# Kernel optimization log

Hardware: AMD Instinct MI355X
Metric: run time of the kernel (lower is better)

Reference implementation:

```python
import jax, jax.numpy as jnp
import numpy as np

LAMBDA1 = 0.3366
LAMBDA2 = 0.2424
LAMBDA3 = 0.06
LR = 0.1
N_ITERS = 10          # fixed iteration count standing in for the eps-based while loop
BETA1, BETA2, ADAM_EPS = 0.9, 0.999, 1e-8


def setup_inputs() -> dict:
    key = jax.random.key(0)
    k1, k2, k3 = jax.random.split(key, 3)
    D, T, K = 512, 50000, 16
    return {
        "embedding": jax.random.normal(k1, (D, T), jnp.float32),
        "basis_init": jax.random.normal(k2, (D, K), jnp.float32),
        "activation_init": jax.random.normal(k3, (K, T), jnp.float32),
        "k": K,
    }


def _matrix_l1(X):
    # torch.linalg.norm(X, ord=1) on a 2D tensor = induced 1-norm = max column abs-sum
    return jnp.max(jnp.sum(jnp.abs(X), axis=0))


def _jitter(A):
    # temporal jitter penalty: sum of abs frame-to-frame differences
    return jnp.sum(jnp.abs(A[:, 1:] - A[:, :-1]))


def _shrink(X):
    # faithful to the (buggy) torch _shrink: sign(X) * max(0, |X - lr*l|)
    return jnp.sign(X) * jnp.maximum(0.0, jnp.abs(X - LR * LAMBDA1))


def _adam(p, g, m, v, t):
    m = BETA1 * m + (1.0 - BETA1) * g
    v = BETA2 * v + (1.0 - BETA2) * g * g
    mh = m / (1.0 - BETA1 ** t)
    vh = v / (1.0 - BETA2 ** t)
    p = p - LR * mh / (jnp.sqrt(vh) + ADAM_EPS)
    return p, m, v


def _run(embedding, basis_init, activation_init):
    A = activation_init  # optimizer_act.step() is never called in the source -> A is constant

    def loss_from_B(B):
        return (_matrix_l1(embedding - B @ A)
                + LAMBDA1 * _matrix_l1(B)
                + LAMBDA2 * _matrix_l1(A)
                + LAMBDA3 * _jitter(A))

    # iteration 1: loss is computed on the raw parameter (shrink applied after the step)
    P = basis_init
    m = jnp.zeros_like(P)
    v = jnp.zeros_like(P)
    g = jax.grad(loss_from_B)(P)
    P, m, v = _adam(P, g, m, v, jnp.float32(1.0))

    # iterations 2..N: loss sees shrink(P); gradient flows through the shrink into P
    def step(carry, t):
        P, m, v = carry
        g = jax.grad(lambda p: loss_from_B(_shrink(p)))(P)
        P, m, v = _adam(P, g, m, v, t)
        return (P, m, v), None

    ts = jnp.arange(2, N_ITERS + 1, dtype=jnp.float32)
    (P, m, v), _ = jax.lax.scan(step, (P, m, v), ts)
    return _shrink(P), A


def reference(embedding, basis_init, activation_init, k):
    # returns (embedding_basis_matrix, activation_matrix) as in OutputDiarization
    return _run(embedding, basis_init, activation_init)
```

## Files before the change

### kernel.cpp

```cpp
#include <hip/hip_runtime.h>

#define D 512
#define T 50000
#define K 16

#define ROWS_PER_SLICE 64
#define N_SLICES (D / ROWS_PER_SLICE)

#define LAMBDA1 0.3366f
#define LR      0.1f
#define SHRINK_C (LR * LAMBDA1)
#define BETA1   0.9f
#define BETA2   0.999f
#define ADAM_EPS 1e-8f

__device__ __forceinline__ float sgn(float x) {
    return (x > 0.f) ? 1.f : ((x < 0.f) ? -1.f : 0.f);
}

__global__ void init_kernel(const float* __restrict__ Pin, float* __restrict__ P,
                            float* __restrict__ m, float* __restrict__ v,
                            float* __restrict__ B, unsigned long long* slot) {
    int idx = blockIdx.x * blockDim.x + threadIdx.x;
    if (idx < D * K) {
        float p = Pin[idx];
        P[idx] = p;
        m[idx] = 0.f;
        v[idx] = 0.f;
        B[idx] = p;
    }
    if (idx == 0) *slot = 0ull;
}

__global__ __launch_bounds__(256) void partial_colsum_kernel(
        const float* __restrict__ E, const float* __restrict__ A,
        const float* __restrict__ B, float* __restrict__ partial) {
    int j = blockIdx.x * blockDim.x + threadIdx.x;
    int s = blockIdx.y;
    if (j >= T) return;

    float a[K];
#pragma unroll
    for (int k = 0; k < K; ++k) a[k] = A[k * T + j];

    int r0 = s * ROWS_PER_SLICE;
    float acc = 0.f;
#pragma unroll 4
    for (int ii = 0; ii < ROWS_PER_SLICE; ++ii) {
        int i = r0 + ii;
        float r = E[i * T + j];
        const float* Br = B + i * K;
#pragma unroll
        for (int k = 0; k < K; ++k) r -= Br[k] * a[k];
        acc += fabsf(r);
    }
    partial[s * T + j] = acc;
}

__global__ __launch_bounds__(256) void reduce_argmax_kernel(
        const float* __restrict__ partial, unsigned long long* slot) {
    int j = blockIdx.x * blockDim.x + threadIdx.x;
    float acc = 0.f;
    if (j < T) {
#pragma unroll
        for (int s = 0; s < N_SLICES; ++s) acc += partial[s * T + j];
    }
    unsigned long long key =
        (((unsigned long long)__float_as_uint(acc)) << 32) | (unsigned int)j;
    if (j >= T) key = 0ull;

#pragma unroll
    for (int off = 32; off > 0; off >>= 1) {
        unsigned long long o = __shfl_down(key, off, 64);
        if (o > key) key = o;
    }
    __shared__ unsigned long long wmax[4];
    int lane = threadIdx.x & 63, wid = threadIdx.x >> 6;
    if (lane == 0) wmax[wid] = key;
    __syncthreads();
    if (threadIdx.x == 0) {
        unsigned long long best = wmax[0];
        for (int w = 1; w < 4; ++w)
            if (wmax[w] > best) best = wmax[w];
        atomicMax(slot, best);
    }
}

__global__ __launch_bounds__(512) void update_kernel(
        const float* __restrict__ E, const float* __restrict__ A,
        float* __restrict__ B, float* __restrict__ P,
        float* __restrict__ m, float* __restrict__ v,
        unsigned long long* slot, float bias1, float bias2, int shrinkGrad) {
    int i = threadIdx.x;
    __shared__ float colB[K];
    __shared__ int js_s, ks_s;
    if (i < K) colB[i] = 0.f;
    if (i == 0) js_s = (int)((*slot) & 0xffffffffull);
    __syncthreads();
    int js = js_s;

    float b[K];
#pragma unroll
    for (int k = 0; k < K; ++k) b[k] = B[i * K + k];

    float r = E[i * T + js];
#pragma unroll
    for (int k = 0; k < K; ++k) r -= b[k] * A[k * T + js];
    float s = sgn(r);

#pragma unroll
    for (int k = 0; k < K; ++k) {
        float x = fabsf(b[k]);
#pragma unroll
        for (int off = 32; off > 0; off >>= 1) x += __shfl_down(x, off, 64);
        if ((threadIdx.x & 63) == 0) atomicAdd(&colB[k], x);
    }
    __syncthreads();
    if (i == 0) {
        int kb = 0;
        float best = colB[0];
        for (int k = 1; k < K; ++k)
            if (colB[k] > best) { best = colB[k]; kb = k; }
        ks_s = kb;
        *slot = 0ull;
    }
    __syncthreads();
    int ks = ks_s;

#pragma unroll
    for (int k = 0; k < K; ++k) {
        float g = -s * A[k * T + js];
        if (k == ks) g += LAMBDA1 * sgn(b[k]);
        float p = P[i * K + k];
        if (shrinkGrad) g *= sgn(p) * sgn(p - SHRINK_C);
        float mm = BETA1 * m[i * K + k] + (1.f - BETA1) * g;
        float vv = BETA2 * v[i * K + k] + (1.f - BETA2) * g * g;
        m[i * K + k] = mm;
        v[i * K + k] = vv;
        p -= LR * (mm / bias1) / (sqrtf(vv / bias2) + ADAM_EPS);
        P[i * K + k] = p;
        B[i * K + k] = sgn(p) * fmaxf(0.f, fabsf(p - SHRINK_C));
    }
}

__global__ void output_kernel(const float* __restrict__ B, const float* __restrict__ A,
                              float4* __restrict__ out) {
    int idx = blockIdx.x * blockDim.x + threadIdx.x;
    const int nB4 = (D * K) / 4;
    const int nTot4 = (D * K + K * T) / 4;
    if (idx < nB4) {
        out[idx] = ((const float4*)B)[idx];
    } else if (idx < nTot4) {
        out[idx] = ((const float4*)A)[idx - nB4];
    }
}

extern "C" void kernel_launch(void* const* d_in, const int* in_sizes, int n_in,
                              void* d_out, int out_size, void* d_ws, size_t ws_size,
                              hipStream_t stream) {
    const float* E   = (const float*)d_in[0];
    const float* Bin = (const float*)d_in[1];
    const float* A   = (const float*)d_in[2];

    float* P = (float*)d_ws;
    float* m = P + D * K;
    float* v = m + D * K;
    float* B = v + D * K;
    unsigned long long* slot = (unsigned long long*)(B + D * K);
    float* partial = (float*)(slot + 2);

    init_kernel<<<(D * K + 255) / 256, 256, 0, stream>>>(Bin, P, m, v, B, slot);

    const int cb = (T + 255) / 256;
    for (int it = 1; it <= 10; ++it) {
        partial_colsum_kernel<<<dim3(cb, N_SLICES), 256, 0, stream>>>(E, A, B, partial);
        reduce_argmax_kernel<<<cb, 256, 0, stream>>>(partial, slot);
        float b1 = 1.f - powf(BETA1, (float)it);
        float b2 = 1.f - powf(BETA2, (float)it);
        update_kernel<<<1, 512, 0, stream>>>(E, A, B, P, m, v, slot, b1, b2,
                                             (it >= 2) ? 1 : 0);
    }

    const int nTot4 = (D * K + K * T) / 4;
    output_kernel<<<(nTot4 + 255) / 256, 256, 0, stream>>>(B, A, (float4*)d_out);
}
```

Measured before the change: 769.7 us.

## Fuse colsum, argmax and Adam update into one last-block-done kernel per iteration

Replaces the three kernels per iteration with a single kernel. Blocks compute float4-vectorized partial column abs-sums over 16 row slices, and the last slice-block per column group reduces the partials and publishes an argmax. The last column group then runs the Adam update, using atomic counters and threadfences instead of kernel boundaries. This cuts launch overhead and the separate reduce pass, but the whole grid is only 49x16 blocks and the final update runs in a single block, serialized at the end of each iteration.

```diff
diff --git a/kernel.cpp b/kernel.cpp
--- a/kernel.cpp
+++ b/kernel.cpp
@@ -2,10 +2,12 @@
 
 #define D 512
 #define T 50000
+#define T4 12500
 #define K 16
 
-#define ROWS_PER_SLICE 64
-#define N_SLICES (D / ROWS_PER_SLICE)
+#define S 16
+#define RS (D / S)
+#define CG 49
 
 #define LAMBDA1 0.3366f
 #define LR      0.1f
@@ -20,7 +22,8 @@
 
 __global__ void init_kernel(const float* __restrict__ Pin, float* __restrict__ P,
                             float* __restrict__ m, float* __restrict__ v,
-                            float* __restrict__ B, unsigned long long* slot) {
+                            float* __restrict__ B, unsigned long long* slot,
+                            int* colDone, int* doneCnt) {
     int idx = blockIdx.x * blockDim.x + threadIdx.x;
     if (idx < D * K) {
         float p = Pin[idx];
@@ -29,118 +32,173 @@
         v[idx] = 0.f;
         B[idx] = p;
     }
-    if (idx == 0) *slot = 0ull;
-}
-
-__global__ __launch_bounds__(256) void partial_colsum_kernel(
+    if (idx < CG) colDone[idx] = 0;
+    if (idx == CG) *doneCnt = 0;
+    if (idx == CG + 1) *slot = 0ull;
+}
+
+__global__ __launch_bounds__(256) void iter_kernel(
         const float* __restrict__ E, const float* __restrict__ A,
-        const float* __restrict__ B, float* __restrict__ partial) {
-    int j = blockIdx.x * blockDim.x + threadIdx.x;
-    int s = blockIdx.y;
-    if (j >= T) return;
-
-    float a[K];
-#pragma unroll
-    for (int k = 0; k < K; ++k) a[k] = A[k * T + j];
-
-    int r0 = s * ROWS_PER_SLICE;
-    float acc = 0.f;
+        float* __restrict__ B, float* __restrict__ P,
+        float* __restrict__ m, float* __restrict__ v,
+        unsigned long long* slot, int* colDone, int* doneCnt,
+        float4* __restrict__ partial4,
+        float bias1, float bias2, int shrinkGrad) {
+    const int tid = threadIdx.x;
+    const int bx  = blockIdx.x;
+    const int s   = blockIdx.y;
+    const int j4  = bx * 256 + tid;
+    const bool active = (j4 < T4);
+
+    const float4* E4 = (const float4*)E;
+    const float4* A4 = (const float4*)A;
+
+    if (active) {
+        float4 a[K];
+#pragma unroll
+        for (int k = 0; k < K; ++k) a[k] = A4[k * T4 + j4];
+
+        float4 acc = make_float4(0.f, 0.f, 0.f, 0.f);
+        const int r0 = s * RS;
 #pragma unroll 4
-    for (int ii = 0; ii < ROWS_PER_SLICE; ++ii) {
-        int i = r0 + ii;
-        float r = E[i * T + j];
-        const float* Br = B + i * K;
-#pragma unroll
-        for (int k = 0; k < K; ++k) r -= Br[k] * a[k];
-        acc += fabsf(r);
-    }
-    partial[s * T + j] = acc;
-}
-
-__global__ __launch_bounds__(256) void reduce_argmax_kernel(
-        const float* __restrict__ partial, unsigned long long* slot) {
-    int j = blockIdx.x * blockDim.x + threadIdx.x;
-    float acc = 0.f;
-    if (j < T) {
-#pragma unroll
-        for (int s = 0; s < N_SLICES; ++s) acc += partial[s * T + j];
-    }
-    unsigned long long key =
-        (((unsigned long long)__float_as_uint(acc)) << 32) | (unsigned int)j;
-    if (j >= T) key = 0ull;
-
+        for (int ii = 0; ii < RS; ++ii) {
+            const int i = r0 + ii;
+            const float* Br = B + i * K;
+            float4 e = E4[i * T4 + j4];
+#pragma unroll
+            for (int k = 0; k < K; ++k) {
+                float bk = Br[k];
+                e.x -= bk * a[k].x;
+                e.y -= bk * a[k].y;
+                e.z -= bk * a[k].z;
+                e.w -= bk * a[k].w;
+            }
+            acc.x += fabsf(e.x);
+            acc.y += fabsf(e.y);
+            acc.z += fabsf(e.z);
+            acc.w += fabsf(e.w);
+        }
+        partial4[s * T4 + j4] = acc;
+    }
+
+    __threadfence();
+    __syncthreads();
+    __shared__ int flag_s;
+    if (tid == 0)
+        flag_s = (atomicAdd(&colDone[bx], 1) == S - 1) ? 1 : 0;
+    __syncthreads();
+    if (!flag_s) return;
+
+    if (tid == 0) __threadfence();
+    __syncthreads();
+
+    unsigned long long key = 0ull;
+    if (active) {
+        float4 sum = make_float4(0.f, 0.f, 0.f, 0.f);
+#pragma unroll
+        for (int ss = 0; ss < S; ++ss) {
+            float4 p = partial4[ss * T4 + j4];
+            sum.x += p.x; sum.y += p.y; sum.z += p.z; sum.w += p.w;
+        }
+        float best = sum.x; int jb = 4 * j4;
+        if (sum.y > best) { best = sum.y; jb = 4 * j4 + 1; }
+        if (sum.z > best) { best = sum.z; jb = 4 * j4 + 2; }
+        if (sum.w > best) { best = sum.w; jb = 4 * j4 + 3; }
+        key = (((unsigned long long)__float_as_uint(best)) << 32) | (unsigned int)jb;
+    }
 #pragma unroll
     for (int off = 32; off > 0; off >>= 1) {
         unsigned long long o = __shfl_down(key, off, 64);
         if (o > key) key = o;
     }
     __shared__ unsigned long long wmax[4];
-    int lane = threadIdx.x & 63, wid = threadIdx.x >> 6;
+    int lane = tid & 63, wid = tid >> 6;
     if (lane == 0) wmax[wid] = key;
     __syncthreads();
-    if (threadIdx.x == 0) {
-        unsigned long long best = wmax[0];
+    if (tid == 0) {
+        unsigned long long bk = wmax[0];
         for (int w = 1; w < 4; ++w)
-            if (wmax[w] > best) best = wmax[w];
-        atomicMax(slot, best);
-    }
-}
-
-__global__ __launch_bounds__(512) void update_kernel(
-        const float* __restrict__ E, const float* __restrict__ A,
-        float* __restrict__ B, float* __restrict__ P,
-        float* __restrict__ m, float* __restrict__ v,
-        unsigned long long* slot, float bias1, float bias2, int shrinkGrad) {
-    int i = threadIdx.x;
+            if (wmax[w] > bk) bk = wmax[w];
+        atomicMax(slot, bk);
+    }
+
+    __threadfence();
+    __syncthreads();
+    if (tid == 0)
+        flag_s = (atomicAdd(doneCnt, 1) == CG - 1) ? 1 : 0;
+    __syncthreads();
+    if (!flag_s) return;
+
+    __shared__ int js_s, ks_s;
     __shared__ float colB[K];
-    __shared__ int js_s, ks_s;
-    if (i < K) colB[i] = 0.f;
-    if (i == 0) js_s = (int)((*slot) & 0xffffffffull);
-    __syncthreads();
-    int js = js_s;
-
-    float b[K];
-#pragma unroll
-    for (int k = 0; k < K; ++k) b[k] = B[i * K + k];
-
-    float r = E[i * T + js];
-#pragma unroll
-    for (int k = 0; k < K; ++k) r -= b[k] * A[k * T + js];
-    float s = sgn(r);
-
+    if (tid == 0) {
+        unsigned long long v0 = atomicMax(slot, 0ull);
+        js_s = (int)(v0 & 0xffffffffull);
+    }
+    if (tid < K) colB[tid] = 0.f;
+    __syncthreads();
+    const int js = js_s;
+
+    const int i0 = tid;
+    const int i1 = tid + 256;
+
+    float b0[K], b1v[K];
+#pragma unroll
+    for (int k = 0; k < K; ++k) { b0[k] = B[i0 * K + k]; b1v[k] = B[i1 * K + k]; }
+
+    float r0v = E[i0 * T + js];
+    float r1v = E[i1 * T + js];
 #pragma unroll
     for (int k = 0; k < K; ++k) {
-        float x = fabsf(b[k]);
+        float ak = A[k * T + js];
+        r0v -= b0[k] * ak;
+        r1v -= b1v[k] * ak;
+    }
+    const float s0 = sgn(r0v), s1 = sgn(r1v);
+
+#pragma unroll
+    for (int k = 0; k < K; ++k) {
+        float x = fabsf(b0[k]) + fabsf(b1v[k]);
 #pragma unroll
         for (int off = 32; off > 0; off >>= 1) x += __shfl_down(x, off, 64);
-        if ((threadIdx.x & 63) == 0) atomicAdd(&colB[k], x);
-    }
-    __syncthreads();
-    if (i == 0) {
+        if ((tid & 63) == 0) atomicAdd(&colB[k], x);
+    }
+    __syncthreads();
+    if (tid == 0) {
         int kb = 0;
         float best = colB[0];
         for (int k = 1; k < K; ++k)
             if (colB[k] > best) { best = colB[k]; kb = k; }
         ks_s = kb;
-        *slot = 0ull;
-    }
-    __syncthreads();
-    int ks = ks_s;
+    }
+    __syncthreads();
+    const int ks = ks_s;
 
 #pragma unroll
     for (int k = 0; k < K; ++k) {
-        float g = -s * A[k * T + js];
-        if (k == ks) g += LAMBDA1 * sgn(b[k]);
-        float p = P[i * K + k];
-        if (shrinkGrad) g *= sgn(p) * sgn(p - SHRINK_C);
-        float mm = BETA1 * m[i * K + k] + (1.f - BETA1) * g;
-        float vv = BETA2 * v[i * K + k] + (1.f - BETA2) * g * g;
-        m[i * K + k] = mm;
-        v[i * K + k] = vv;
-        p -= LR * (mm / bias1) / (sqrtf(vv / bias2) + ADAM_EPS);
-        P[i * K + k] = p;
-        B[i * K + k] = sgn(p) * fmaxf(0.f, fabsf(p - SHRINK_C));
-    }
+        float ak = A[k * T + js];
+#pragma unroll
+        for (int h = 0; h < 2; ++h) {
+            const int i = h ? i1 : i0;
+            const float sg = h ? s1 : s0;
+            const float bk = h ? b1v[k] : b0[k];
+            float g = -sg * ak;
+            if (k == ks) g += LAMBDA1 * sgn(bk);
+            float p = P[i * K + k];
+            if (shrinkGrad) g *= sgn(p) * sgn(p - SHRINK_C);
+            float mm = BETA1 * m[i * K + k] + (1.f - BETA1) * g;
+            float vv = BETA2 * v[i * K + k] + (1.f - BETA2) * g * g;
+            m[i * K + k] = mm;
+            v[i * K + k] = vv;
+            p -= LR * (mm / bias1) / (sqrtf(vv / bias2) + ADAM_EPS);
+            P[i * K + k] = p;
+            B[i * K + k] = sgn(p) * fmaxf(0.f, fabsf(p - SHRINK_C));
+        }
+    }
+
+    if (tid < CG) colDone[tid] = 0;
+    if (tid == CG) *doneCnt = 0;
+    if (tid == CG + 1) *slot = 0ull;
 }
 
 __global__ void output_kernel(const float* __restrict__ B, const float* __restrict__ A,
@@ -167,18 +225,19 @@
     float* v = m + D * K;
     float* B = v + D * K;
     unsigned long long* slot = (unsigned long long*)(B + D * K);
-    float* partial = (float*)(slot + 2);
-
-    init_kernel<<<(D * K + 255) / 256, 256, 0, stream>>>(Bin, P, m, v, B, slot);
-
-    const int cb = (T + 255) / 256;
+    int* colDone = (int*)(slot + 2);
+    int* doneCnt = colDone + CG;
+    float4* partial4 = (float4*)((char*)d_ws + ((4u * D * K + 64u + CG + 8u) * 4u + 127u & ~127u));
+
+    init_kernel<<<(D * K + 255) / 256, 256, 0, stream>>>(Bin, P, m, v, B, slot,
+                                                         colDone, doneCnt);
+
     for (int it = 1; it <= 10; ++it) {
-        partial_colsum_kernel<<<dim3(cb, N_SLICES), 256, 0, stream>>>(E, A, B, partial);
-        reduce_argmax_kernel<<<cb, 256, 0, stream>>>(partial, slot);
         float b1 = 1.f - powf(BETA1, (float)it);
         float b2 = 1.f - powf(BETA2, (float)it);
-        update_kernel<<<1, 512, 0, stream>>>(E, A, B, P, m, v, slot, b1, b2,
-                                             (it >= 2) ? 1 : 0);
+        iter_kernel<<<dim3(CG, S), 256, 0, stream>>>(E, A, B, P, m, v, slot,
+                                                     colDone, doneCnt, partial4,
+                                                     b1, b2, (it >= 2) ? 1 : 0);
     }
 
     const int nTot4 = (D * K + K * T) / 4;
```

Result: slower. 1.781 ms (+131.4%).

## Vectorize column-sum kernel with float4 per thread and use 32 row slices

Applied to the files above, without the earlier changes.

Each thread in the residual column-sum kernel now handles four adjacent columns with float4 loads of E and A. Each B coefficient load is reused across four columns and memory transactions get wider. The row dimension is split into 32 slices instead of 8 to keep enough blocks in flight now that there are 4x fewer column threads. The reduce kernel sums the 32 float4 partials and takes a per-thread argmax over four columns before the wave reduction. In exchange it holds 64 float registers for A and writes more partial-sum traffic.

```diff
diff --git a/kernel.cpp b/kernel.cpp
--- a/kernel.cpp
+++ b/kernel.cpp
@@ -2,10 +2,12 @@
 
 #define D 512
 #define T 50000
+#define T4 12500
 #define K 16
 
-#define ROWS_PER_SLICE 64
-#define N_SLICES (D / ROWS_PER_SLICE)
+#define S 32
+#define RS (D / S)
+#define CB 49
 
 #define LAMBDA1 0.3366f
 #define LR      0.1f
@@ -34,55 +36,72 @@
 
 __global__ __launch_bounds__(256) void partial_colsum_kernel(
         const float* __restrict__ E, const float* __restrict__ A,
-        const float* __restrict__ B, float* __restrict__ partial) {
-    int j = blockIdx.x * blockDim.x + threadIdx.x;
-    int s = blockIdx.y;
-    if (j >= T) return;
-
-    float a[K];
-#pragma unroll
-    for (int k = 0; k < K; ++k) a[k] = A[k * T + j];
-
-    int r0 = s * ROWS_PER_SLICE;
-    float acc = 0.f;
+        const float* __restrict__ B, float4* __restrict__ partial4) {
+    const int j4 = blockIdx.x * blockDim.x + threadIdx.x;
+    const int s  = blockIdx.y;
+    if (j4 >= T4) return;
+
+    const float4* E4 = (const float4*)E;
+    const float4* A4 = (const float4*)A;
+
+    float4 a[K];
+#pragma unroll
+    for (int k = 0; k < K; ++k) a[k] = A4[k * T4 + j4];
+
+    float4 acc = make_float4(0.f, 0.f, 0.f, 0.f);
+    const int r0 = s * RS;
 #pragma unroll 4
-    for (int ii = 0; ii < ROWS_PER_SLICE; ++ii) {
-        int i = r0 + ii;
-        float r = E[i * T + j];
+    for (int ii = 0; ii < RS; ++ii) {
+        const int i = r0 + ii;
         const float* Br = B + i * K;
-#pragma unroll
-        for (int k = 0; k < K; ++k) r -= Br[k] * a[k];
-        acc += fabsf(r);
-    }
-    partial[s * T + j] = acc;
+        float4 e = E4[i * T4 + j4];
+#pragma unroll
+        for (int k = 0; k < K; ++k) {
+            const float bk = Br[k];
+            e.x -= bk * a[k].x;
+            e.y -= bk * a[k].y;
+            e.z -= bk * a[k].z;
+            e.w -= bk * a[k].w;
+        }
+        acc.x += fabsf(e.x);
+        acc.y += fabsf(e.y);
+        acc.z += fabsf(e.z);
+        acc.w += fabsf(e.w);
+    }
+    partial4[s * T4 + j4] = acc;
 }
 
 __global__ __launch_bounds__(256) void reduce_argmax_kernel(
-        const float* __restrict__ partial, unsigned long long* slot) {
-    int j = blockIdx.x * blockDim.x + threadIdx.x;
-    float acc = 0.f;
-    if (j < T) {
-#pragma unroll
-        for (int s = 0; s < N_SLICES; ++s) acc += partial[s * T + j];
-    }
-    unsigned long long key =
-        (((unsigned long long)__float_as_uint(acc)) << 32) | (unsigned int)j;
-    if (j >= T) key = 0ull;
-
+        const float4* __restrict__ partial4, unsigned long long* slot) {
+    const int j4 = blockIdx.x * blockDim.x + threadIdx.x;
+    unsigned long long key = 0ull;
+    if (j4 < T4) {
+        float4 sum = make_float4(0.f, 0.f, 0.f, 0.f);
+#pragma unroll
+        for (int ss = 0; ss < S; ++ss) {
+            float4 p = partial4[ss * T4 + j4];
+            sum.x += p.x; sum.y += p.y; sum.z += p.z; sum.w += p.w;
+        }
+        float best = sum.x; int jb = 4 * j4;
+        if (sum.y > best) { best = sum.y; jb = 4 * j4 + 1; }
+        if (sum.z > best) { best = sum.z; jb = 4 * j4 + 2; }
+        if (sum.w > best) { best = sum.w; jb = 4 * j4 + 3; }
+        key = (((unsigned long long)__float_as_uint(best)) << 32) | (unsigned int)jb;
+    }
 #pragma unroll
     for (int off = 32; off > 0; off >>= 1) {
         unsigned long long o = __shfl_down(key, off, 64);
         if (o > key) key = o;
     }
     __shared__ unsigned long long wmax[4];
-    int lane = threadIdx.x & 63, wid = threadIdx.x >> 6;
+    const int lane = threadIdx.x & 63, wid = threadIdx.x >> 6;
     if (lane == 0) wmax[wid] = key;
     __syncthreads();
     if (threadIdx.x == 0) {
-        unsigned long long best = wmax[0];
+        unsigned long long bk = wmax[0];
         for (int w = 1; w < 4; ++w)
-            if (wmax[w] > best) best = wmax[w];
-        atomicMax(slot, best);
+            if (wmax[w] > bk) bk = wmax[w];
+        atomicMax(slot, bk);
     }
 }
 
@@ -167,14 +186,13 @@
     float* v = m + D * K;
     float* B = v + D * K;
     unsigned long long* slot = (unsigned long long*)(B + D * K);
-    float* partial = (float*)(slot + 2);
+    float4* partial4 = (float4*)(slot + 2);
 
     init_kernel<<<(D * K + 255) / 256, 256, 0, stream>>>(Bin, P, m, v, B, slot);
 
-    const int cb = (T + 255) / 256;
     for (int it = 1; it <= 10; ++it) {
-        partial_colsum_kernel<<<dim3(cb, N_SLICES), 256, 0, stream>>>(E, A, B, partial);
-        reduce_argmax_kernel<<<cb, 256, 0, stream>>>(partial, slot);
+        partial_colsum_kernel<<<dim3(CB, S), 256, 0, stream>>>(E, A, B, partial4);
+        reduce_argmax_kernel<<<CB, 256, 0, stream>>>(partial4, slot);
         float b1 = 1.f - powf(BETA1, (float)it);
         float b2 = 1.f - powf(BETA2, (float)it);
         update_kernel<<<1, 512, 0, stream>>>(E, A, B, P, m, v, slot, b1, b2,
```

New measurement: 789.7 us. +2.6%, slower.
